# Performance work log

Hardware: AMD Instinct MI355X
Metric: run time of the kernel (lower is better)

Reference implementation:

```python
import jax, jax.numpy as jnp
import numpy as np

D_MODEL = 1024
NUM_HEADS = 16
D_K = D_MODEL // NUM_HEADS
B, S = 1, 2048


def _rope(x, sin, cos):
    # x: [B,H,S,d_k]; sin/cos: [S, d_k//2] broadcast over B,H
    xe = x[..., 0::2]
    xo = x[..., 1::2]
    out_e = xe * cos - xo * sin
    out_o = xe * sin + xo * cos
    return jnp.stack([out_e, out_o], axis=-1).reshape(x.shape)


def setup_inputs() -> dict:
    key = jax.random.key(0)
    ks = jax.random.split(key, 12)
    sc = 1.0 / np.sqrt(D_MODEL)
    inp = {
        "Q": jax.random.normal(ks[0], (B, S, D_MODEL), jnp.float32),
        "K": jax.random.normal(ks[1], (B, S, D_MODEL), jnp.float32),
        "V": jax.random.normal(ks[2], (B, S, D_MODEL), jnp.float32),
        "position_ids": jnp.arange(S, dtype=jnp.int32),
        "mask": jnp.tril(jnp.ones((S, S), dtype=bool))[None, None],  # causal [1,1,S,S]
        "W_q": jax.random.normal(ks[3], (D_MODEL, D_MODEL), jnp.float32) * sc,
        "b_q": jnp.zeros((D_MODEL,), jnp.float32),
        "W_k": jax.random.normal(ks[4], (D_MODEL, D_MODEL), jnp.float32) * sc,
        "b_k": jnp.zeros((D_MODEL,), jnp.float32),
        "W_v": jax.random.normal(ks[5], (D_MODEL, D_MODEL), jnp.float32) * sc,
        "b_v": jnp.zeros((D_MODEL,), jnp.float32),
        "W_o": jax.random.normal(ks[6], (D_MODEL, D_MODEL), jnp.float32) * sc,
        "b_o": jnp.zeros((D_MODEL,), jnp.float32),
    }
    return inp


def reference(Q, K, V, position_ids, mask, W_q, b_q, W_k, b_k, W_v, b_v, W_o, b_o):
    b = Q.shape[0]
    # QKV projections (torch Linear: x @ W.T + b), split into heads [B,H,S,d_k]
    def proj(x, W, bias):
        y = jnp.einsum('bsd,ed->bse', x, W) + bias
        return y.reshape(b, -1, NUM_HEADS, D_K).transpose(0, 2, 1, 3)

    q = proj(Q, W_q, b_q)
    k = proj(K, W_k, b_k)
    v = proj(V, W_v, b_v)

    # rotary: theta_i = 10000^(-2i/d_model), first d_k/2 frequencies
    theta = 10000.0 ** (-2.0 * jnp.arange(D_K // 2, dtype=jnp.float32) / D_MODEL)
    angles = position_ids.astype(jnp.float32)[:, None] * theta  # [S, d_k/2]
    sin, cos = jnp.sin(angles), jnp.cos(angles)
    q = _rope(q, sin, cos)
    k = _rope(k, sin, cos)

    scores = jnp.einsum('bhqd,bhkd->bhqk', q, k) / np.sqrt(D_K)
    scores = jnp.where(mask, scores, jnp.float32(-1e9))
    attn = jax.nn.softmax(scores, axis=-1)
    out = jnp.einsum('bhqk,bhkd->bhqd', attn, v)
    out = out.transpose(0, 2, 1, 3).reshape(b, -1, D_MODEL)
    out = jnp.einsum('bsd,ed->bse', out, W_o) + b_o
    return (out, attn)
```

## Files before the change

kernel.cpp:

```cpp
#include <hip/hip_runtime.h>
#include <hip/hip_bf16.h>

#define S_LEN 2048
#define DMODEL 1024
#define NHEADS 16
#define DHEAD 64

typedef short bf16x8 __attribute__((ext_vector_type(8)));
typedef float f32x4 __attribute__((ext_vector_type(4)));

__device__ __forceinline__ unsigned short f2bf(float f) {
    unsigned int u = __builtin_bit_cast(unsigned int, f);
    u = u + 0x7fffu + ((u >> 16) & 1u);
    return (unsigned short)(u >> 16);
}
__device__ __forceinline__ unsigned short f2bf_trunc(float f) {
    return (unsigned short)(__builtin_bit_cast(unsigned int, f) >> 16);
}
__device__ __forceinline__ bf16x8 ldfrag(const unsigned short* p) {
    return *reinterpret_cast<const bf16x8*>(p);
}
__device__ __forceinline__ bf16x8 ld8cvt(const float* p) {
    const float4 u = *reinterpret_cast<const float4*>(p);
    const float4 v = *reinterpret_cast<const float4*>(p + 4);
    bf16x8 r;
    r[0] = (short)f2bf(u.x); r[1] = (short)f2bf(u.y);
    r[2] = (short)f2bf(u.z); r[3] = (short)f2bf(u.w);
    r[4] = (short)f2bf(v.x); r[5] = (short)f2bf(v.y);
    r[6] = (short)f2bf(v.z); r[7] = (short)f2bf(v.w);
    return r;
}

__device__ __forceinline__ void gload_lds16(const unsigned short* g, unsigned short* l) {
    __builtin_amdgcn_global_load_lds(
        (const __attribute__((address_space(1))) unsigned int*)(const void*)g,
        (__attribute__((address_space(3))) unsigned int*)(unsigned int)(uintptr_t)(void*)l,
        16, 0, 0);
}

#define EXP2_C1 0.18033688011112042f
#define EXP2_C0 -11.541560327111707f

__global__ __launch_bounds__(256) void k_cvt(
    const float* __restrict__ Q, const float* __restrict__ K, const float* __restrict__ V,
    const float* __restrict__ Wq, const float* __restrict__ Wk, const float* __restrict__ Wv,
    const float* __restrict__ Wo,
    unsigned short* __restrict__ Xb, unsigned short* __restrict__ Wb)
{
    size_t i4 = (size_t)blockIdx.x * blockDim.x + threadIdx.x;
    size_t e  = i4 << 2;
    const float* s; unsigned short* d;
    if      (e < 2097152) { s = Q  + e;             d = Xb + e; }
    else if (e < 4194304) { s = K  + (e - 2097152); d = Xb + e; }
    else if (e < 6291456) { s = V  + (e - 4194304); d = Xb + e; }
    else if (e < 7340032) { s = Wq + (e - 6291456); d = Wb + (e - 6291456); }
    else if (e < 8388608) { s = Wk + (e - 7340032); d = Wb + (e - 6291456); }
    else if (e < 9437184) { s = Wv + (e - 8388608); d = Wb + (e - 6291456); }
    else                  { s = Wo + (e - 9437184); d = Wb + (e - 6291456); }
    float4 v4 = *reinterpret_cast<const float4*>(s);
    unsigned int lo = (unsigned)f2bf(v4.x) | ((unsigned)f2bf(v4.y) << 16);
    unsigned int hi = (unsigned)f2bf(v4.z) | ((unsigned)f2bf(v4.w) << 16);
    *reinterpret_cast<uint2*>(d) = make_uint2(lo, hi);
}

__device__ __forceinline__ void stage_tile64(const unsigned short* __restrict__ A,
                                             const unsigned short* __restrict__ B,
                                             unsigned short* buf, int k0, int tid)
{
    int q = tid;
    int row = q >> 2;
    int cc = (q & 3) ^ (row & 3) ^ ((row >> 2) & 3);
    const unsigned short* srcA = A + (size_t)row * DMODEL + k0 + cc * 8;
    const unsigned short* srcB = B + (size_t)row * DMODEL + k0 + cc * 8;
    unsigned short* dstbase = buf + (size_t)(tid & ~63) * 8;
    gload_lds16(srcA, dstbase);
    gload_lds16(srcB, dstbase + 2048);
}

__device__ __forceinline__ void gemm_mainloop64(const unsigned short* __restrict__ A,
                                                const unsigned short* __restrict__ B,
                                                unsigned short (*lds)[4096],
                                                f32x4 acc[2][2])
{
    int tid = threadIdx.x;
    int w = tid >> 6, lane = tid & 63;
    int lr = lane & 15, lg = lane >> 4;
    int wr = w >> 1, wc = w & 1;

    #pragma unroll
    for (int tm = 0; tm < 2; ++tm)
        #pragma unroll
        for (int tn = 0; tn < 2; ++tn) acc[tm][tn] = (f32x4){0.f, 0.f, 0.f, 0.f};

    stage_tile64(A, B, lds[0], 0, tid);
    __syncthreads();
    int cur = 0;
    for (int ks = 0; ks < 32; ++ks) {
        if (ks < 31) stage_tile64(A, B, lds[cur ^ 1], (ks + 1) * 32, tid);
        bf16x8 af[2], bfr[2];
        #pragma unroll
        for (int t = 0; t < 2; ++t) {
            int rowA = wr * 32 + t * 16 + lr;
            int cc = lg ^ (rowA & 3) ^ ((rowA >> 2) & 3);
            af[t] = ldfrag(&lds[cur][(size_t)rowA * 32 + cc * 8]);
        }
        #pragma unroll
        for (int t = 0; t < 2; ++t) {
            int rowB = wc * 32 + t * 16 + lr;
            int cc = lg ^ (rowB & 3) ^ ((rowB >> 2) & 3);
            bfr[t] = ldfrag(&lds[cur][2048 + (size_t)rowB * 32 + cc * 8]);
        }
        #pragma unroll
        for (int tm = 0; tm < 2; ++tm)
            #pragma unroll
            for (int tn = 0; tn < 2; ++tn)
                acc[tm][tn] = __builtin_amdgcn_mfma_f32_16x16x32_bf16(af[tm], bfr[tn], acc[tm][tn], 0, 0, 0);
        __syncthreads();
        cur ^= 1;
    }
}

__global__ __launch_bounds__(256, 6) void k_proj2(
    const unsigned short* __restrict__ Xb, const unsigned short* __restrict__ Wb,
    const float* __restrict__ bq, const float* __restrict__ bk, const float* __restrict__ bv,
    const int* __restrict__ pos,
    unsigned short* __restrict__ qh, unsigned short* __restrict__ kh,
    unsigned short* __restrict__ vT)
{
    __shared__ unsigned short lds[2][4096];
    int b0 = blockIdx.x;
    int bid = (b0 & 7) * 192 + (b0 >> 3);
    int z = bid >> 9;
    int rem = bid & 511;
    int bm = rem >> 4, bn = rem & 15;

    const unsigned short* A = Xb + (size_t)z * S_LEN * DMODEL + (size_t)bm * 64 * DMODEL;
    const unsigned short* B = Wb + (size_t)z * DMODEL * DMODEL + (size_t)bn * 64 * DMODEL;

    f32x4 acc[2][2];
    gemm_mainloop64(A, B, lds, acc);

    int lane = threadIdx.x & 63;
    int w = threadIdx.x >> 6;
    int lr = lane & 15, lg = lane >> 4;
    int wr = w >> 1, wc = w & 1;
    const float* bias_ = (z == 0) ? bq : (z == 1) ? bk : bv;

    if (z == 2) {
        #pragma unroll
        for (int tm = 0; tm < 2; ++tm) {
            int sbase = bm * 64 + wr * 32 + tm * 16 + lg * 4;
            #pragma unroll
            for (int tn = 0; tn < 2; ++tn) {
                int e = bn * 64 + wc * 32 + tn * 16 + lr;
                float bv_ = bias_[e];
                unsigned int lo = (unsigned)f2bf(acc[tm][tn][0] + bv_) | ((unsigned)f2bf(acc[tm][tn][1] + bv_) << 16);
                unsigned int hi = (unsigned)f2bf(acc[tm][tn][2] + bv_) | ((unsigned)f2bf(acc[tm][tn][3] + bv_) << 16);
                *reinterpret_cast<uint2*>(vT + (size_t)e * S_LEN + sbase) = make_uint2(lo, hi);
            }
        }
    } else {
        unsigned short* dstp = (z == 0) ? qh : kh;
        #pragma unroll
        for (int tm = 0; tm < 2; ++tm) {
            #pragma unroll
            for (int tn = 0; tn < 2; ++tn) {
                int e = bn * 64 + wc * 32 + tn * 16 + lr;
                float bv_ = bias_[e];
                int dk = e & 63, h = e >> 6, p = dk >> 1;
                float theta = __expf((float)p * -0.017988946039015984f);
                #pragma unroll
                for (int r = 0; r < 4; ++r) {
                    float y  = acc[tm][tn][r] + bv_;
                    float yp = __shfl_xor(y, 1);
                    int srow = bm * 64 + wr * 32 + tm * 16 + lg * 4 + r;
                    float ang = (float)pos[srow] * theta;
                    float sv, cv;
                    sincosf(ang, &sv, &cv);
                    float o = fmaf(y, cv, (dk & 1) ? yp * sv : -(yp * sv));
                    dstp[(size_t)(h * S_LEN + srow) * DHEAD + dk] = f2bf(o);
                }
            }
        }
    }
}

__global__ __launch_bounds__(256, 6) void k_out2(
    const unsigned short* __restrict__ outh, const unsigned short* __restrict__ Wob,
    const float* __restrict__ bo, float* __restrict__ out)
{
    __shared__ unsigned short lds[2][4096];
    int b0 = blockIdx.x;
    int bid = (b0 & 7) * 64 + (b0 >> 3);
    int bm = bid >> 4, bn = bid & 15;
    const unsigned short* A = outh + (size_t)bm * 64 * DMODEL;
    const unsigned short* B = Wob + (size_t)bn * 64 * DMODEL;

    f32x4 acc[2][2];
    gemm_mainloop64(A, B, lds, acc);

    int lane = threadIdx.x & 63;
    int w = threadIdx.x >> 6;
    int lr = lane & 15, lg = lane >> 4;
    int wr = w >> 1, wc = w & 1;

    #pragma unroll
    for (int tm = 0; tm < 2; ++tm) {
        #pragma unroll
        for (int tn = 0; tn < 2; ++tn) {
            int e = bn * 64 + wc * 32 + tn * 16 + lr;
            float bv_ = bo[e];
            #pragma unroll
            for (int r = 0; r < 4; ++r) {
                int srow = bm * 64 + wr * 32 + tm * 16 + lg * 4 + r;
                out[(size_t)srow * DMODEL + e] = acc[tm][tn][r] + bv_;
            }
        }
    }
}

__global__ __launch_bounds__(256) void k_attn5(
    const unsigned short* __restrict__ qh, const unsigned short* __restrict__ kh,
    const unsigned short* __restrict__ vT,
    float* __restrict__ attnf, unsigned short* __restrict__ outh)
{
    __shared__ float po[4][16][64];
    __shared__ float sl[4][16];
    __shared__ unsigned short plds[4][16 * 40];

    int w    = threadIdx.x >> 6;
    int lane = threadIdx.x & 63;
    int bid  = blockIdx.x;
    int xcd  = bid & 7;
    int j    = bid >> 3;
    int h    = xcd * 2 + (j & 1);
    int qb   = 127 - (j >> 1);
    int s0   = qb << 4;
    int lr   = lane & 15, lg = lane >> 4;
    unsigned short* P = plds[w];
    float* sstage = &po[w][0][0];

    int nkb = qb + 1;
    int kb0 = (nkb * w) >> 2;
    int kb1 = (nkb * (w + 1)) >> 2;

    const unsigned short* qrow = qh + (size_t)(h * S_LEN + s0 + lr) * DHEAD + lg * 8;
    bf16x8 aq0 = ldfrag(qrow);
    bf16x8 aq1 = ldfrag(qrow + 32);

    float l_[4];
    #pragma unroll
    for (int r = 0; r < 4; ++r) l_[r] = 0.f;

    for (int kb = kb0; kb < kb1; ++kb) {
        const unsigned short* krow = kh + (size_t)(h * S_LEN + kb * 16 + lr) * DHEAD + lg * 8;
        f32x4 acc = (f32x4){0.f, 0.f, 0.f, 0.f};
        acc = __builtin_amdgcn_mfma_f32_16x16x32_bf16(aq0, ldfrag(krow),      acc, 0, 0, 0);
        acc = __builtin_amdgcn_mfma_f32_16x16x32_bf16(aq1, ldfrag(krow + 32), acc, 0, 0, 0);
        bool diag = (kb == qb);
        #pragma unroll
        for (int r = 0; r < 4; ++r) {
            float e = __builtin_amdgcn_exp2f(fmaf(acc[r], EXP2_C1, EXP2_C0));
            if (diag && lr > lg * 4 + r) e = 0.f;
            l_[r] += e;
        }
    }
    #pragma unroll
    for (int msk = 1; msk < 16; msk <<= 1)
        #pragma unroll
        for (int r = 0; r < 4; ++r)
            l_[r] += __shfl_xor(l_[r], msk);
    if (lr == 0) {
        #pragma unroll
        for (int r = 0; r < 4; ++r) sl[w][lg * 4 + r] = l_[r];
    }
    __syncthreads();

    float invl[4];
    #pragma unroll
    for (int r = 0; r < 4; ++r) {
        int row = lg * 4 + r;
        invl[r] = 1.0f / (sl[0][row] + sl[1][row] + sl[2][row] + sl[3][row]);
    }

    f32x4 oacc[4];
    #pragma unroll
    for (int t = 0; t < 4; ++t) oacc[t] = (f32x4){0.f, 0.f, 0.f, 0.f};

    int srow_st = lane >> 3;
    int scol_st = (lane & 7) * 4;

    for (int kb2 = kb0; kb2 < kb1; kb2 += 2) {
        bool full = (kb2 + 1 < kb1);
        #pragma unroll
        for (int sub = 0; sub < 2; ++sub) {
            int kb = kb2 + sub;
            float pv[4];
            if (kb < kb1) {
                const unsigned short* krow = kh + (size_t)(h * S_LEN + kb * 16 + lr) * DHEAD + lg * 8;
                f32x4 acc = (f32x4){0.f, 0.f, 0.f, 0.f};
                acc = __builtin_amdgcn_mfma_f32_16x16x32_bf16(aq0, ldfrag(krow),      acc, 0, 0, 0);
                acc = __builtin_amdgcn_mfma_f32_16x16x32_bf16(aq1, ldfrag(krow + 32), acc, 0, 0, 0);
                bool diag = (kb == qb);
                #pragma unroll
                for (int r = 0; r < 4; ++r) {
                    pv[r] = __builtin_amdgcn_exp2f(fmaf(acc[r], EXP2_C1, EXP2_C0)) * invl[r];
                    if (diag && lr > lg * 4 + r) pv[r] = 0.f;
                }
            } else {
                #pragma unroll
                for (int r = 0; r < 4; ++r) pv[r] = 0.f;
            }
            #pragma unroll
            for (int r = 0; r < 4; ++r) {
                sstage[(lg * 4 + r) * 33 + sub * 16 + lr] = pv[r];
                P[(lg * 4 + r) * 40 + sub * 16 + lr] = f2bf_trunc(pv[r]);
            }
        }
        if (full || scol_st < 16) {
            f32x4 v0 = *reinterpret_cast<const f32x4*>(&sstage[srow_st * 33 + scol_st]);
            f32x4 v1 = *reinterpret_cast<const f32x4*>(&sstage[(srow_st + 8) * 33 + scol_st]);
            size_t base = (size_t)(h * S_LEN + s0) * S_LEN + kb2 * 16 + scol_st;
            __builtin_nontemporal_store(v0, reinterpret_cast<f32x4*>(&attnf[base + (size_t)srow_st * S_LEN]));
            __builtin_nontemporal_store(v1, reinterpret_cast<f32x4*>(&attnf[base + (size_t)(srow_st + 8) * S_LEN]));
        }
        bf16x8 a = ldfrag(&P[lr * 40 + lg * 8]);
        int k0 = kb2 * 16;
        #pragma unroll
        for (int t = 0; t < 4; ++t) {
            bf16x8 b = ldfrag(vT + (size_t)(h * DHEAD + t * 16 + lr) * S_LEN + k0 + lg * 8);
            oacc[t] = __builtin_amdgcn_mfma_f32_16x16x32_bf16(a, b, oacc[t], 0, 0, 0);
        }
    }

    #pragma unroll
    for (int t = 0; t < 4; ++t)
        #pragma unroll
        for (int r = 0; r < 4; ++r)
            po[w][lg * 4 + r][t * 16 + lr] = oacc[t][r];

    int zs = (qb + 1) * 16;
    f32x4 z4 = (f32x4){0.f, 0.f, 0.f, 0.f};
    #pragma unroll
    for (int i = 0; i < 4; ++i) {
        float* row = attnf + (size_t)(h * S_LEN + s0 + w * 4 + i) * S_LEN;
        for (int c = zs + lane * 4; c < S_LEN; c += 256)
            __builtin_nontemporal_store(z4, reinterpret_cast<f32x4*>(row + c));
    }
    __syncthreads();

    for (int e = threadIdx.x; e < 1024; e += 256) {
        int row = e >> 6, col = e & 63;
        float s = po[0][row][col] + po[1][row][col] + po[2][row][col] + po[3][row][col];
        outh[(size_t)(s0 + row) * DMODEL + h * DHEAD + col] = f2bf(s);
    }
}

__global__ __launch_bounds__(256) void k_proj_legacy(
    const float* __restrict__ Q, const float* __restrict__ Kin,
    const float* __restrict__ V,
    const float* __restrict__ Wq, const float* __restrict__ bq,
    const float* __restrict__ Wk, const float* __restrict__ bk,
    const float* __restrict__ Wv, const float* __restrict__ bv,
    const int* __restrict__ pos,
    unsigned short* __restrict__ qh, unsigned short* __restrict__ kh,
    unsigned short* __restrict__ vT)
{
    int w    = (blockIdx.x * blockDim.x + threadIdx.x) >> 6;
    int lane = threadIdx.x & 63;
    int z    = w >> 11;
    int rem  = w & 2047;
    int mt   = rem >> 4;
    int ns   = rem & 15;
    int s0   = mt << 4;
    int e0   = ns << 6;
    int lr   = lane & 15, lg = lane >> 4;

    const float* X     = (z == 0) ? Q  : (z == 1) ? Kin : V;
    const float* W     = (z == 0) ? Wq : (z == 1) ? Wk  : Wv;
    const float* bias_ = (z == 0) ? bq : (z == 1) ? bk  : bv;

    f32x4 acc[4];
    #pragma unroll
    for (int t = 0; t < 4; ++t) acc[t] = (f32x4){0.f, 0.f, 0.f, 0.f};

    const float* arow = X + (size_t)(s0 + lr) * DMODEL + lg * 8;
    const float* brow = W + (size_t)(e0 + lr) * DMODEL + lg * 8;

    for (int kk = 0; kk < 32; ++kk) {
        int koff = kk * 32;
        bf16x8 a = ld8cvt(arow + koff);
        #pragma unroll
        for (int t = 0; t < 4; ++t) {
            bf16x8 b = ld8cvt(brow + (size_t)t * 16 * DMODEL + koff);
            acc[t] = __builtin_amdgcn_mfma_f32_16x16x32_bf16(a, b, acc[t], 0, 0, 0);
        }
    }

    if (z == 2) {
        #pragma unroll
        for (int t = 0; t < 4; ++t) {
            int e = e0 + t * 16 + lr;
            float bv_ = bias_[e];
            int sbase = s0 + lg * 4;
            unsigned int lo = (unsigned)f2bf(acc[t][0] + bv_) | ((unsigned)f2bf(acc[t][1] + bv_) << 16);
            unsigned int hi = (unsigned)f2bf(acc[t][2] + bv_) | ((unsigned)f2bf(acc[t][3] + bv_) << 16);
            *reinterpret_cast<uint2*>(vT + (size_t)e * S_LEN + sbase) = make_uint2(lo, hi);
        }
    } else {
        unsigned short* dstp = (z == 0) ? qh : kh;
        #pragma unroll
        for (int t = 0; t < 4; ++t) {
            int e = e0 + t * 16 + lr;
            float bv_ = bias_[e];
            int dk = e & 63, h = e >> 6, p = dk >> 1;
            float theta = __expf((float)p * -0.017988946039015984f);
            #pragma unroll
            for (int r = 0; r < 4; ++r) {
                float y  = acc[t][r] + bv_;
                float yp = __shfl_xor(y, 1);
                int srow = s0 + lg * 4 + r;
                float ang = (float)pos[srow] * theta;
                float sv, cv;
                sincosf(ang, &sv, &cv);
                float o = fmaf(y, cv, (dk & 1) ? yp * sv : -(yp * sv));
                dstp[(size_t)(h * S_LEN + srow) * DHEAD + dk] = f2bf(o);
            }
        }
    }
}

__global__ __launch_bounds__(256) void k_out_legacy(
    const unsigned short* __restrict__ outh, const float* __restrict__ Wo,
    const float* __restrict__ bo, float* __restrict__ out)
{
    int w    = (blockIdx.x * blockDim.x + threadIdx.x) >> 6;
    int lane = threadIdx.x & 63;
    int mt   = w >> 4, ns = w & 15;
    int s0   = mt << 4, e0 = ns << 6;
    int lr   = lane & 15, lg = lane >> 4;

    f32x4 acc[4];
    #pragma unroll
    for (int t = 0; t < 4; ++t) acc[t] = (f32x4){0.f, 0.f, 0.f, 0.f};

    const unsigned short* arow = outh + (size_t)(s0 + lr) * DMODEL + lg * 8;
    const float* brow = Wo + (size_t)(e0 + lr) * DMODEL + lg * 8;

    for (int kk = 0; kk < 32; ++kk) {
        int koff = kk * 32;
        bf16x8 a = ldfrag(arow + koff);
        #pragma unroll
        for (int t = 0; t < 4; ++t) {
            bf16x8 b = ld8cvt(brow + (size_t)t * 16 * DMODEL + koff);
            acc[t] = __builtin_amdgcn_mfma_f32_16x16x32_bf16(a, b, acc[t], 0, 0, 0);
        }
    }
    #pragma unroll
    for (int t = 0; t < 4; ++t) {
        int e = e0 + t * 16 + lr;
        float bv_ = bo[e];
        #pragma unroll
        for (int r = 0; r < 4; ++r)
            out[(size_t)(s0 + lg * 4 + r) * DMODEL + e] = acc[t][r] + bv_;
    }
}

extern "C" void kernel_launch(void* const* d_in, const int* in_sizes, int n_in,
                              void* d_out, int out_size, void* d_ws, size_t ws_size,
                              hipStream_t stream)
{
    const float* Q   = (const float*)d_in[0];
    const float* K   = (const float*)d_in[1];
    const float* V   = (const float*)d_in[2];
    const int*   pos = (const int*)d_in[3];
    const float* Wq = (const float*)d_in[5];
    const float* bq = (const float*)d_in[6];
    const float* Wk = (const float*)d_in[7];
    const float* bk = (const float*)d_in[8];
    const float* Wv = (const float*)d_in[9];
    const float* bv = (const float*)d_in[10];
    const float* Wo = (const float*)d_in[11];
    const float* bo = (const float*)d_in[12];

    float* out   = (float*)d_out;
    float* attnf = out + (size_t)S_LEN * DMODEL;

    char* ws = (char*)d_ws;
    unsigned short* qh = (unsigned short*)ws;
    unsigned short* kh = (unsigned short*)(ws + (4u << 20));
    unsigned short* vT = (unsigned short*)(ws + (8u << 20));

    const size_t OUTH_OFF = (size_t)(13u << 20);
    const size_t WB_OFF   = OUTH_OFF + (4u << 20);
    const size_t XB_OFF   = WB_OFF + (8u << 20);
    const size_t BASE_END = XB_OFF + (12u << 20);
    bool newpath = (ws_size >= BASE_END);

    if (newpath) {
        unsigned short* outh = (unsigned short*)(ws + OUTH_OFF);
        unsigned short* Wb   = (unsigned short*)(ws + WB_OFF);
        unsigned short* Xb   = (unsigned short*)(ws + XB_OFF);
        unsigned short* Wob  = Wb + (size_t)3 * DMODEL * DMODEL;

        k_cvt  <<<10240, 256, 0, stream>>>(Q, K, V, Wq, Wk, Wv, Wo, Xb, Wb);
        k_proj2<<<1536, 256, 0, stream>>>(Xb, Wb, bq, bk, bv, pos, qh, kh, vT);
        k_attn5<<<2048, 256, 0, stream>>>(qh, kh, vT, attnf, outh);
        k_out2 <<<512, 256, 0, stream>>>(outh, Wob, bo, out);
    } else {
        unsigned short* outh = (unsigned short*)(ws + (12u << 20));
        k_proj_legacy<<<1536, 256, 0, stream>>>(Q, K, V, Wq, bq, Wk, bk, Wv, bv, pos, qh, kh, vT);
        k_attn5<<<2048, 256, 0, stream>>>(qh, kh, vT, attnf, outh);
        k_out_legacy<<<512, 256, 0, stream>>>(outh, Wo, bo, out);
    }
}
```

Before: 167.6 us.

## Process 32 query rows per attention block to reuse K/V fragments

The attention kernel now handles two 16-row query tiles per block, so each K and V fragment load feeds two MFMAs, and the grid is halved. The fp32 staging buffer for the attention-probability stores is dropped. Probabilities are written from the bf16 LDS tile, and the partial outputs are reduced through bf16 LDS, which shrinks shared memory. The cost is that stored attention probabilities are truncated to bf16 precision, partial sums are rounded to bf16, and there are fewer blocks with more causal-imbalance work per block.

```diff
diff --git a/kernel.cpp b/kernel.cpp
--- a/kernel.cpp
+++ b/kernel.cpp
@@ -16,6 +16,10 @@
 }
 __device__ __forceinline__ unsigned short f2bf_trunc(float f) {
     return (unsigned short)(__builtin_bit_cast(unsigned int, f) >> 16);
+}
+__device__ __forceinline__ float bf2f(unsigned short h) {
+    unsigned int u = ((unsigned int)h) << 16;
+    return __builtin_bit_cast(float, u);
 }
 __device__ __forceinline__ bf16x8 ldfrag(const unsigned short* p) {
     return *reinterpret_cast<const bf16x8*>(p);
@@ -219,14 +223,13 @@
     }
 }
 
-__global__ __launch_bounds__(256) void k_attn5(
+__global__ __launch_bounds__(256) void k_attn6(
     const unsigned short* __restrict__ qh, const unsigned short* __restrict__ kh,
     const unsigned short* __restrict__ vT,
     float* __restrict__ attnf, unsigned short* __restrict__ outh)
 {
-    __shared__ float po[4][16][64];
-    __shared__ float sl[4][16];
-    __shared__ unsigned short plds[4][16 * 40];
+    __shared__ unsigned short pbuf[4][2048];
+    __shared__ float sl[4][32];
 
     int w    = threadIdx.x >> 6;
     int lane = threadIdx.x & 63;
@@ -234,124 +237,162 @@
     int xcd  = bid & 7;
     int j    = bid >> 3;
     int h    = xcd * 2 + (j & 1);
-    int qb   = 127 - (j >> 1);
-    int s0   = qb << 4;
+    int qt   = 63 - (j >> 1);
+    int s0   = qt << 5;
+    int qb0  = qt * 2, qb1 = qb0 + 1;
     int lr   = lane & 15, lg = lane >> 4;
-    unsigned short* P = plds[w];
-    float* sstage = &po[w][0][0];
-
-    int nkb = qb + 1;
+    unsigned short* P = pbuf[w];
+
+    int nkb = qb1 + 1;
     int kb0 = (nkb * w) >> 2;
     int kb1 = (nkb * (w + 1)) >> 2;
 
-    const unsigned short* qrow = qh + (size_t)(h * S_LEN + s0 + lr) * DHEAD + lg * 8;
-    bf16x8 aq0 = ldfrag(qrow);
-    bf16x8 aq1 = ldfrag(qrow + 32);
-
-    float l_[4];
-    #pragma unroll
-    for (int r = 0; r < 4; ++r) l_[r] = 0.f;
+    const unsigned short* qrow0 = qh + (size_t)(h * S_LEN + s0 + lr) * DHEAD + lg * 8;
+    const unsigned short* qrow1 = qh + (size_t)(h * S_LEN + s0 + 16 + lr) * DHEAD + lg * 8;
+    bf16x8 aq00 = ldfrag(qrow0), aq01 = ldfrag(qrow0 + 32);
+    bf16x8 aq10 = ldfrag(qrow1), aq11 = ldfrag(qrow1 + 32);
+
+    float l0_[4], l1_[4];
+    #pragma unroll
+    for (int r = 0; r < 4; ++r) { l0_[r] = 0.f; l1_[r] = 0.f; }
 
     for (int kb = kb0; kb < kb1; ++kb) {
         const unsigned short* krow = kh + (size_t)(h * S_LEN + kb * 16 + lr) * DHEAD + lg * 8;
-        f32x4 acc = (f32x4){0.f, 0.f, 0.f, 0.f};
-        acc = __builtin_amdgcn_mfma_f32_16x16x32_bf16(aq0, ldfrag(krow),      acc, 0, 0, 0);
-        acc = __builtin_amdgcn_mfma_f32_16x16x32_bf16(aq1, ldfrag(krow + 32), acc, 0, 0, 0);
-        bool diag = (kb == qb);
+        bf16x8 k0f = ldfrag(krow), k1f = ldfrag(krow + 32);
+        f32x4 acc0 = (f32x4){0.f, 0.f, 0.f, 0.f};
+        f32x4 acc1 = (f32x4){0.f, 0.f, 0.f, 0.f};
+        acc0 = __builtin_amdgcn_mfma_f32_16x16x32_bf16(aq00, k0f, acc0, 0, 0, 0);
+        acc1 = __builtin_amdgcn_mfma_f32_16x16x32_bf16(aq10, k0f, acc1, 0, 0, 0);
+        acc0 = __builtin_amdgcn_mfma_f32_16x16x32_bf16(aq01, k1f, acc0, 0, 0, 0);
+        acc1 = __builtin_amdgcn_mfma_f32_16x16x32_bf16(aq11, k1f, acc1, 0, 0, 0);
+        bool d0 = (kb == qb0), z0 = (kb == qb1), d1 = (kb == qb1);
         #pragma unroll
         for (int r = 0; r < 4; ++r) {
-            float e = __builtin_amdgcn_exp2f(fmaf(acc[r], EXP2_C1, EXP2_C0));
-            if (diag && lr > lg * 4 + r) e = 0.f;
-            l_[r] += e;
+            float e0 = __builtin_amdgcn_exp2f(fmaf(acc0[r], EXP2_C1, EXP2_C0));
+            if ((d0 && lr > lg * 4 + r) || z0) e0 = 0.f;
+            l0_[r] += e0;
+            float e1 = __builtin_amdgcn_exp2f(fmaf(acc1[r], EXP2_C1, EXP2_C0));
+            if (d1 && lr > lg * 4 + r) e1 = 0.f;
+            l1_[r] += e1;
         }
     }
     #pragma unroll
     for (int msk = 1; msk < 16; msk <<= 1)
         #pragma unroll
-        for (int r = 0; r < 4; ++r)
-            l_[r] += __shfl_xor(l_[r], msk);
+        for (int r = 0; r < 4; ++r) {
+            l0_[r] += __shfl_xor(l0_[r], msk);
+            l1_[r] += __shfl_xor(l1_[r], msk);
+        }
     if (lr == 0) {
         #pragma unroll
-        for (int r = 0; r < 4; ++r) sl[w][lg * 4 + r] = l_[r];
+        for (int r = 0; r < 4; ++r) {
+            sl[w][lg * 4 + r]      = l0_[r];
+            sl[w][16 + lg * 4 + r] = l1_[r];
+        }
     }
     __syncthreads();
 
-    float invl[4];
+    float invl0[4], invl1[4];
     #pragma unroll
     for (int r = 0; r < 4; ++r) {
-        int row = lg * 4 + r;
-        invl[r] = 1.0f / (sl[0][row] + sl[1][row] + sl[2][row] + sl[3][row]);
-    }
-
-    f32x4 oacc[4];
-    #pragma unroll
-    for (int t = 0; t < 4; ++t) oacc[t] = (f32x4){0.f, 0.f, 0.f, 0.f};
-
-    int srow_st = lane >> 3;
-    int scol_st = (lane & 7) * 4;
+        int r0 = lg * 4 + r, r1 = 16 + lg * 4 + r;
+        invl0[r] = 1.0f / (sl[0][r0] + sl[1][r0] + sl[2][r0] + sl[3][r0]);
+        invl1[r] = 1.0f / (sl[0][r1] + sl[1][r1] + sl[2][r1] + sl[3][r1]);
+    }
+
+    f32x4 oacc0[4], oacc1[4];
+    #pragma unroll
+    for (int t = 0; t < 4; ++t) {
+        oacc0[t] = (f32x4){0.f, 0.f, 0.f, 0.f};
+        oacc1[t] = (f32x4){0.f, 0.f, 0.f, 0.f};
+    }
+
+    int row_st = lane >> 1;
+    int col_st = (lane & 1) << 4;
 
     for (int kb2 = kb0; kb2 < kb1; kb2 += 2) {
         bool full = (kb2 + 1 < kb1);
         #pragma unroll
         for (int sub = 0; sub < 2; ++sub) {
             int kb = kb2 + sub;
-            float pv[4];
+            float pv0[4], pv1[4];
             if (kb < kb1) {
                 const unsigned short* krow = kh + (size_t)(h * S_LEN + kb * 16 + lr) * DHEAD + lg * 8;
-                f32x4 acc = (f32x4){0.f, 0.f, 0.f, 0.f};
-                acc = __builtin_amdgcn_mfma_f32_16x16x32_bf16(aq0, ldfrag(krow),      acc, 0, 0, 0);
-                acc = __builtin_amdgcn_mfma_f32_16x16x32_bf16(aq1, ldfrag(krow + 32), acc, 0, 0, 0);
-                bool diag = (kb == qb);
+                bf16x8 k0f = ldfrag(krow), k1f = ldfrag(krow + 32);
+                f32x4 acc0 = (f32x4){0.f, 0.f, 0.f, 0.f};
+                f32x4 acc1 = (f32x4){0.f, 0.f, 0.f, 0.f};
+                acc0 = __builtin_amdgcn_mfma_f32_16x16x32_bf16(aq00, k0f, acc0, 0, 0, 0);
+                acc1 = __builtin_amdgcn_mfma_f32_16x16x32_bf16(aq10, k0f, acc1, 0, 0, 0);
+                acc0 = __builtin_amdgcn_mfma_f32_16x16x32_bf16(aq01, k1f, acc0, 0, 0, 0);
+                acc1 = __builtin_amdgcn_mfma_f32_16x16x32_bf16(aq11, k1f, acc1, 0, 0, 0);
+                bool d0 = (kb == qb0), z0 = (kb == qb1), d1 = (kb == qb1);
                 #pragma unroll
                 for (int r = 0; r < 4; ++r) {
-                    pv[r] = __builtin_amdgcn_exp2f(fmaf(acc[r], EXP2_C1, EXP2_C0)) * invl[r];
-                    if (diag && lr > lg * 4 + r) pv[r] = 0.f;
+                    pv0[r] = __builtin_amdgcn_exp2f(fmaf(acc0[r], EXP2_C1, EXP2_C0)) * invl0[r];
+                    if ((d0 && lr > lg * 4 + r) || z0) pv0[r] = 0.f;
+                    pv1[r] = __builtin_amdgcn_exp2f(fmaf(acc1[r], EXP2_C1, EXP2_C0)) * invl1[r];
+                    if (d1 && lr > lg * 4 + r) pv1[r] = 0.f;
                 }
             } else {
                 #pragma unroll
-                for (int r = 0; r < 4; ++r) pv[r] = 0.f;
+                for (int r = 0; r < 4; ++r) { pv0[r] = 0.f; pv1[r] = 0.f; }
             }
             #pragma unroll
             for (int r = 0; r < 4; ++r) {
-                sstage[(lg * 4 + r) * 33 + sub * 16 + lr] = pv[r];
-                P[(lg * 4 + r) * 40 + sub * 16 + lr] = f2bf_trunc(pv[r]);
-            }
-        }
-        if (full || scol_st < 16) {
-            f32x4 v0 = *reinterpret_cast<const f32x4*>(&sstage[srow_st * 33 + scol_st]);
-            f32x4 v1 = *reinterpret_cast<const f32x4*>(&sstage[(srow_st + 8) * 33 + scol_st]);
-            size_t base = (size_t)(h * S_LEN + s0) * S_LEN + kb2 * 16 + scol_st;
-            __builtin_nontemporal_store(v0, reinterpret_cast<f32x4*>(&attnf[base + (size_t)srow_st * S_LEN]));
-            __builtin_nontemporal_store(v1, reinterpret_cast<f32x4*>(&attnf[base + (size_t)(srow_st + 8) * S_LEN]));
-        }
-        bf16x8 a = ldfrag(&P[lr * 40 + lg * 8]);
+                P[(lg * 4 + r) * 40 + sub * 16 + lr]        = f2bf_trunc(pv0[r]);
+                P[(16 + lg * 4 + r) * 40 + sub * 16 + lr]   = f2bf_trunc(pv1[r]);
+            }
+        }
+        if (full || col_st == 0) {
+            bf16x8 u0 = ldfrag(&P[row_st * 40 + col_st]);
+            bf16x8 u1 = ldfrag(&P[row_st * 40 + col_st + 8]);
+            f32x4 v0, v1, v2, v3;
+            #pragma unroll
+            for (int i = 0; i < 4; ++i) {
+                v0[i] = bf2f((unsigned short)u0[i]);
+                v1[i] = bf2f((unsigned short)u0[i + 4]);
+                v2[i] = bf2f((unsigned short)u1[i]);
+                v3[i] = bf2f((unsigned short)u1[i + 4]);
+            }
+            float* base = attnf + (size_t)(h * S_LEN + s0 + row_st) * S_LEN + kb2 * 16 + col_st;
+            __builtin_nontemporal_store(v0, reinterpret_cast<f32x4*>(base));
+            __builtin_nontemporal_store(v1, reinterpret_cast<f32x4*>(base + 4));
+            __builtin_nontemporal_store(v2, reinterpret_cast<f32x4*>(base + 8));
+            __builtin_nontemporal_store(v3, reinterpret_cast<f32x4*>(base + 12));
+        }
+        bf16x8 a0 = ldfrag(&P[lr * 40 + lg * 8]);
+        bf16x8 a1 = ldfrag(&P[(16 + lr) * 40 + lg * 8]);
         int k0 = kb2 * 16;
         #pragma unroll
         for (int t = 0; t < 4; ++t) {
             bf16x8 b = ldfrag(vT + (size_t)(h * DHEAD + t * 16 + lr) * S_LEN + k0 + lg * 8);
-            oacc[t] = __builtin_amdgcn_mfma_f32_16x16x32_bf16(a, b, oacc[t], 0, 0, 0);
+            oacc0[t] = __builtin_amdgcn_mfma_f32_16x16x32_bf16(a0, b, oacc0[t], 0, 0, 0);
+            oacc1[t] = __builtin_amdgcn_mfma_f32_16x16x32_bf16(a1, b, oacc1[t], 0, 0, 0);
         }
     }
 
     #pragma unroll
     for (int t = 0; t < 4; ++t)
         #pragma unroll
-        for (int r = 0; r < 4; ++r)
-            po[w][lg * 4 + r][t * 16 + lr] = oacc[t][r];
-
-    int zs = (qb + 1) * 16;
+        for (int r = 0; r < 4; ++r) {
+            P[(lg * 4 + r) * 64 + t * 16 + lr]        = f2bf(oacc0[t][r]);
+            P[(16 + lg * 4 + r) * 64 + t * 16 + lr]   = f2bf(oacc1[t][r]);
+        }
+
+    int zs = s0 + 32;
     f32x4 z4 = (f32x4){0.f, 0.f, 0.f, 0.f};
     #pragma unroll
-    for (int i = 0; i < 4; ++i) {
-        float* row = attnf + (size_t)(h * S_LEN + s0 + w * 4 + i) * S_LEN;
+    for (int i = 0; i < 8; ++i) {
+        float* row = attnf + (size_t)(h * S_LEN + s0 + w * 8 + i) * S_LEN;
         for (int c = zs + lane * 4; c < S_LEN; c += 256)
             __builtin_nontemporal_store(z4, reinterpret_cast<f32x4*>(row + c));
     }
     __syncthreads();
 
-    for (int e = threadIdx.x; e < 1024; e += 256) {
+    for (int e = threadIdx.x; e < 2048; e += 256) {
         int row = e >> 6, col = e & 63;
-        float s = po[0][row][col] + po[1][row][col] + po[2][row][col] + po[3][row][col];
+        float s = bf2f(pbuf[0][row * 64 + col]) + bf2f(pbuf[1][row * 64 + col])
+                + bf2f(pbuf[2][row * 64 + col]) + bf2f(pbuf[3][row * 64 + col]);
         outh[(size_t)(s0 + row) * DMODEL + h * DHEAD + col] = f2bf(s);
     }
 }
@@ -505,12 +546,12 @@
 
         k_cvt  <<<10240, 256, 0, stream>>>(Q, K, V, Wq, Wk, Wv, Wo, Xb, Wb);
         k_proj2<<<1536, 256, 0, stream>>>(Xb, Wb, bq, bk, bv, pos, qh, kh, vT);
-        k_attn5<<<2048, 256, 0, stream>>>(qh, kh, vT, attnf, outh);
+        k_attn6<<<1024, 256, 0, stream>>>(qh, kh, vT, attnf, outh);
         k_out2 <<<512, 256, 0, stream>>>(outh, Wob, bo, out);
     } else {
         unsigned short* outh = (unsigned short*)(ws + (12u << 20));
         k_proj_legacy<<<1536, 256, 0, stream>>>(Q, K, V, Wq, bq, Wk, bk, Wv, bv, pos, qh, kh, vT);
-        k_attn5<<<2048, 256, 0, stream>>>(qh, kh, vT, attnf, outh);
+        k_attn6<<<1024, 256, 0, stream>>>(qh, kh, vT, attnf, outh);
         k_out_legacy<<<512, 256, 0, stream>>>(outh, Wo, bo, out);
     }
 }
```

New measurement: 342.8 us. 2.05x slower.
